# Kernel tuning notes

Hardware: AMD Instinct MI355X
Metric: run time of the kernel (lower is better)

The kernel has to match this reference:

```python
import jax, jax.numpy as jnp
import numpy as np

ALPHA = 0.8
TOPK = 9
LOW_BOUND = 0.0
EPS = 1e-10
IOU_EPS = 1e-6


def pairwise_iou(boxes1, boxes2):
    # boxes1 [N,4], boxes2 [G,4] in x1,y1,x2,y2 -> IoU [N,G] (mmdet BboxOverlaps2D)
    area1 = (boxes1[:, 2] - boxes1[:, 0]) * (boxes1[:, 3] - boxes1[:, 1])  # [N]
    area2 = (boxes2[:, 2] - boxes2[:, 0]) * (boxes2[:, 3] - boxes2[:, 1])  # [G]
    lt = jnp.maximum(boxes1[:, None, :2], boxes2[None, :, :2])  # [N,G,2]
    rb = jnp.minimum(boxes1[:, None, 2:], boxes2[None, :, 2:])  # [N,G,2]
    wh = jnp.clip(rb - lt, 0.0)
    inter = wh[..., 0] * wh[..., 1]  # [N,G]
    union = area1[:, None] + area2[None, :] - inter
    return inter / jnp.maximum(union, IOU_EPS)


def setup_inputs() -> dict:
    key = jax.random.key(0)
    k1, k2, k3, k4, k5, k6, k7 = jax.random.split(key, 7)
    N, G, C = 65536, 256, 80
    IMG = 1024.0
    points = jax.random.uniform(k1, (N, 2), dtype=jnp.float32) * IMG  # (cy, cx)
    p_xy1 = jax.random.uniform(k2, (N, 2), dtype=jnp.float32) * (IMG - 96.0)
    p_wh = jax.random.uniform(k3, (N, 2), dtype=jnp.float32) * 95.0 + 1.0
    bbox_preds = jnp.concatenate([p_xy1, p_xy1 + p_wh], axis=1)  # valid x1y1x2y2
    g_xy1 = jax.random.uniform(k4, (G, 2), dtype=jnp.float32) * (IMG - 256.0)
    g_wh = jax.random.uniform(k5, (G, 2), dtype=jnp.float32) * 255.0 + 1.0
    gt_bboxes = jnp.concatenate([g_xy1, g_xy1 + g_wh], axis=1)
    cls_scores = jax.random.normal(k6, (N, C), dtype=jnp.float32)
    gt_labels = jax.random.randint(k7, (G,), 0, C)
    return {"points": points, "cls_scores": cls_scores, "bbox_preds": bbox_preds,
            "gt_bboxes": gt_bboxes, "gt_labels": gt_labels}


def reference(points, cls_scores, bbox_preds, gt_bboxes, gt_labels):
    num_points = points.shape[0]
    num_gt = gt_bboxes.shape[0]
    overlaps = pairwise_iou(bbox_preds, gt_bboxes)  # [N,G]
    cls_cost = jax.nn.sigmoid(cls_scores[:, gt_labels])  # [N,G]
    overlaps = cls_cost ** (1.0 - ALPHA) * overlaps ** ALPHA
    # top-k points per GT (torch: overlaps.topk(k, dim=0))
    _, topk_idxs = jax.lax.top_k(overlaps.T, TOPK)  # [G,K]
    candidate_idxs = topk_idxs.T  # [K,G]
    cp = jnp.transpose(points[candidate_idxs], (1, 0, 2))  # [G,K,2] (cy,cx)
    # mle_2d_gaussian_2: per-GT MLE Gaussian over candidate points
    miu = cp.mean(axis=1, keepdims=True)  # [G,1,2]
    diff = cp - miu  # [G,K,2]
    sigma = jnp.einsum('gki,gkj->gij', diff, diff) / TOPK  # [G,2,2]
    a, b = sigma[:, 0, 0], sigma[:, 0, 1]
    c, d = sigma[:, 1, 0], sigma[:, 1, 1]
    det = a * d - b * c  # [G]
    inv = jnp.stack([jnp.stack([d, -b], axis=-1),
                     jnp.stack([-c, a], axis=-1)], axis=-2) / (det + EPS)[:, None, None]
    maha = jnp.einsum('gki,gij,gkj->gk', diff, inv, diff)  # [G,K]
    candidate_w = jnp.exp(-0.5 * maha).T  # [K,G]
    # center-inside-gt validity, evaluated only at candidate points
    cy, cx = cp[:, :, 0], cp[:, :, 1]  # [G,K]
    gx1, gy1, gx2, gy2 = (gt_bboxes[:, i][:, None] for i in range(4))  # [G,1]
    valid = ((cx - gx1 > EPS) & (cy - gy1 > EPS) &
             (gx2 - cx > EPS) & (gy2 - cy > EPS)).T  # [K,G]
    wv = candidate_w * valid.astype(candidate_w.dtype)
    # scatter per-GT weights to points, then max over GTs == scatter-max
    w = jnp.zeros((num_points,), dtype=cls_scores.dtype)
    w = w.at[candidate_idxs.reshape(-1)].max(wv.reshape(-1))
    w = jnp.where(w < LOW_BOUND, jnp.zeros_like(w), w)
    return w
```

## Files before the change

kernel.cpp:

```cpp
#include <hip/hip_runtime.h>
#include <hip/hip_bf16.h>
#include <math.h>

#define NPTS   65536
#define NGT    256
#define NCLS   80
#define TOPK   9
#define GSLICE 32
#define NPB    256
#define NXB    (NPTS / NPB)
#define SCAP   64

__device__ inline unsigned long long pack_key(float L, unsigned idx) {
    unsigned u   = __float_as_uint(L);
    unsigned k32 = (u & 0x80000000u) ? ~u : (u | 0x80000000u);
    return ((unsigned long long)k32 << 32) | (unsigned)(~idx);
}

__device__ inline unsigned long long umax64(unsigned long long a,
                                            unsigned long long b) {
    return a > b ? a : b;
}

__device__ inline unsigned long long wave_max64(unsigned long long m) {
#pragma unroll
    for (int off = 1; off < 64; off <<= 1)
        m = umax64(m, (unsigned long long)__shfl_xor(m, off));
    return m;
}

__global__ __launch_bounds__(256) void filter_kernel(
    const float* __restrict__ preds,
    const float* __restrict__ gtb,
    const int*   __restrict__ glab,
    const float* __restrict__ cls,
    unsigned short* __restrict__ counts,
    unsigned long long* __restrict__ bucket,
    float* __restrict__ w)
{
    __shared__ unsigned lcnt[GSLICE];
    __shared__ int      glabs[GSLICE];
    __shared__ unsigned long long stage[GSLICE][SCAP];

    const int t   = threadIdx.x;
    const int xb  = blockIdx.x;
    const int g0  = blockIdx.y * GSLICE;
    const int pt  = xb * NPB + t;
    const int bid = blockIdx.y * NXB + xb;

    if (t < GSLICE) {
        lcnt[t]  = 0u;
        glabs[t] = glab[g0 + t];
    }
    if (t < 32) w[bid * 32 + t] = 0.0f;

    float4 pb = ((const float4*)preds)[pt];
    float parea = (pb.z - pb.x) * (pb.w - pb.y);
    __syncthreads();

    for (int gi = 0; gi < GSLICE; ++gi) {
        const float4 g4 = ((const float4*)gtb)[g0 + gi];
        float ix1 = fmaxf(pb.x, g4.x), iy1 = fmaxf(pb.y, g4.y);
        float ix2 = fminf(pb.z, g4.z), iy2 = fminf(pb.w, g4.w);
        float iw  = fmaxf(ix2 - ix1, 0.0f);
        float ih  = fmaxf(iy2 - iy1, 0.0f);
        float inter = iw * ih;
        if (inter > 0.0f) {
            float garea = (g4.z - g4.x) * (g4.w - g4.y);
            float uni = fmaxf(parea + garea - inter, 1e-6f);
            float iou = inter / uni;
            unsigned long long entry =
                ((unsigned long long)__float_as_uint(iou) << 32) |
                (unsigned)(~(unsigned)pt);
            unsigned slot = atomicAdd(&lcnt[gi], 1u);
            if (slot < SCAP) stage[gi][slot] = entry;
        }
    }
    __syncthreads();

    if (t < GSLICE) {
        unsigned c = lcnt[t];
        if (c > SCAP) c = SCAP;
        lcnt[t] = c;
        counts[(size_t)(g0 + t) * NXB + xb] = (unsigned short)c;
    }
    __syncthreads();

    const float E1 = 1.0f - 0.8f;
#pragma unroll
    for (int k = 0; k < 8; k += 4) {
        unsigned long long e[4];
        bool  vld[4];
        int   gi[4];
        float x[4];
#pragma unroll
        for (int j = 0; j < 4; ++j) {
            int i = (k + j) * 256 + t;
            gi[j] = i >> 6;
            int sl = i & (SCAP - 1);
            e[j]   = stage[gi[j]][sl];
            vld[j] = sl < (int)lcnt[gi[j]];
        }
#pragma unroll
        for (int j = 0; j < 4; ++j) {
            if (vld[j]) {
                unsigned p = ~(unsigned)(e[j] & 0xFFFFFFFFu);
                x[j] = cls[(size_t)p * NCLS + glabs[gi[j]]];
            }
        }
#pragma unroll
        for (int j = 0; j < 4; ++j) {
            if (vld[j]) {
                float iou = __uint_as_float((unsigned)(e[j] >> 32));
                float s   = 1.0f / (1.0f + expf(-x[j]));
                float L   = E1 * log2f(s) + 0.8f * log2f(iou);
                unsigned u   = __float_as_uint(L);
                unsigned k32 = (u & 0x80000000u) ? ~u : (u | 0x80000000u);
                int i = (k + j) * 256 + t;
                bucket[((size_t)(g0 + gi[j]) * NXB + xb) * SCAP + (i & (SCAP - 1))]
                    = ((unsigned long long)k32 << 32) | (e[j] & 0xFFFFFFFFu);
            }
        }
    }
}

__global__ __launch_bounds__(1024) void select_kernel(
    const unsigned short*     __restrict__ counts,
    const unsigned long long* __restrict__ bucket,
    const float* __restrict__ pts,
    const float* __restrict__ gtb,
    float* __restrict__ w)
{
    const int g    = blockIdx.x;
    const int t    = threadIdx.x;
    const int lane = t & 63;
    const int wid  = t >> 6;

    __shared__ unsigned short scnt[NXB];
    __shared__ unsigned long long wl[16 * TOPK];
    __shared__ unsigned tidx[TOPK];
    __shared__ float ppy[TOPK], ppx[TOPK];

    if (t < NXB) scnt[t] = counts[(size_t)g * NXB + t];
    __syncthreads();

    const unsigned long long* src =
        bucket + (size_t)g * (NXB * SCAP) + (size_t)wid * 1024;

    unsigned long long e[16];
#pragma unroll
    for (int k = 0; k < 16; k += 4) {
        unsigned long long v[4];
#pragma unroll
        for (int j = 0; j < 4; ++j) v[j] = src[(k + j) * 64 + lane];
#pragma unroll
        for (int j = 0; j < 4; ++j) {
            int c = (int)scnt[wid * 16 + k + j];
            e[k + j] = (lane < c) ? v[j] : 0ULL;
        }
    }
    unsigned long long mymax = 0ULL;
#pragma unroll
    for (int j = 0; j < 16; ++j) mymax = umax64(mymax, e[j]);

#pragma unroll
    for (int r = 0; r < TOPK; ++r) {
        unsigned long long m = wave_max64(mymax);
        if (lane == 0) wl[wid * TOPK + r] = m;
        if (m != 0ULL && mymax == m) {
#pragma unroll
            for (int j = 0; j < 16; ++j) if (e[j] == m) e[j] = 0ULL;
            mymax = 0ULL;
#pragma unroll
            for (int j = 0; j < 16; ++j) mymax = umax64(mymax, e[j]);
        }
    }
    __syncthreads();

    if (wid == 0) {
        unsigned long long f[4];
        f[0] = wl[lane];
        f[1] = wl[64 + lane];
        f[2] = (lane < 16) ? wl[128 + lane] : 0ULL;
        f[3] = (lane < TOPK) ? pack_key(-INFINITY, (unsigned)lane) : 0ULL;

        unsigned long long mx = 0ULL;
#pragma unroll
        for (int j = 0; j < 4; ++j) mx = umax64(mx, f[j]);

#pragma unroll
        for (int r = 0; r < TOPK; ++r) {
            unsigned long long m = wave_max64(mx);
            if (lane == 0) tidx[r] = ~(unsigned)(m & 0xFFFFFFFFu);
            if (mx == m) {
#pragma unroll
                for (int j = 0; j < 4; ++j) if (f[j] == m) f[j] = 0ULL;
                mx = 0ULL;
#pragma unroll
                for (int j = 0; j < 4; ++j) mx = umax64(mx, f[j]);
            }
        }
    }
    __syncthreads();

    if (t < TOPK) {
        unsigned pi = tidx[t];
        ppy[t] = pts[2 * (size_t)pi];
        ppx[t] = pts[2 * (size_t)pi + 1];
    }
    __syncthreads();

    if (t == 0) {
        float4 g4 = ((const float4*)gtb)[g];
        float m0 = 0.0f, m1 = 0.0f;
#pragma unroll
        for (int k = 0; k < TOPK; ++k) { m0 += ppy[k]; m1 += ppx[k]; }
        m0 /= (float)TOPK; m1 /= (float)TOPK;

        float d0[TOPK], d1[TOPK];
        float a = 0.0f, bb = 0.0f, dd = 0.0f;
#pragma unroll
        for (int k = 0; k < TOPK; ++k) {
            d0[k] = ppy[k] - m0;
            d1[k] = ppx[k] - m1;
            a  += d0[k] * d0[k];
            bb += d0[k] * d1[k];
            dd += d1[k] * d1[k];
        }
        a /= (float)TOPK; bb /= (float)TOPK; dd /= (float)TOPK;
        float det  = a * dd - bb * bb;
        float rinv = 1.0f / (det + 1e-10f);

#pragma unroll
        for (int k = 0; k < TOPK; ++k) {
            float q = d0[k] * (dd * d0[k] - bb * d1[k])
                    + d1[k] * (a  * d1[k] - bb * d0[k]);
            float maha = q * rinv;
            float wt = expf(-0.5f * maha);
            bool valid = (ppx[k] - g4.x > 1e-10f) && (ppy[k] - g4.y > 1e-10f) &&
                         (g4.z - ppx[k] > 1e-10f) && (g4.w - ppy[k] > 1e-10f);
            float wv = valid ? wt : 0.0f;
            atomicMax((int*)&w[tidx[k]], __float_as_int(wv));
        }
    }
}

extern "C" void kernel_launch(void* const* d_in, const int* in_sizes, int n_in,
                              void* d_out, int out_size, void* d_ws, size_t ws_size,
                              hipStream_t stream) {
    const float* points  = (const float*)d_in[0];
    const float* cls     = (const float*)d_in[1];
    const float* preds   = (const float*)d_in[2];
    const float* gtb     = (const float*)d_in[3];
    const int*   glab    = (const int*)d_in[4];
    float* w = (float*)d_out;

    char* ws = (char*)d_ws;
    unsigned long long* bucket = (unsigned long long*)ws;
    size_t off = (size_t)NGT * NXB * SCAP * sizeof(unsigned long long);
    unsigned short* counts = (unsigned short*)(ws + off);

    filter_kernel<<<dim3(NXB, NGT / GSLICE), 256, 0, stream>>>(
        preds, gtb, glab, cls, counts, bucket, w);
    select_kernel<<<NGT, 1024, 0, stream>>>(counts, bucket, points, gtb, w);
}
```

Baseline: 114.6 us.

## Split per-GT top-k selection across four blocks with last-block merge

The select kernel now runs 256-thread blocks, four per ground-truth box, instead of one 1024-thread block per box. Each block picks a local top-9 from a quarter of the buckets and writes it to a workspace buffer. An atomic counter then lets the last-arriving block merge the partial results and compute the Gaussian weights. This raises block count and occupancy for a grid of only 256 blocks, at the cost of extra global traffic, memory fences and an atomic handoff, plus a counter reset done inside the filter kernel.

```diff
diff --git a/kernel.cpp b/kernel.cpp
--- a/kernel.cpp
+++ b/kernel.cpp
@@ -10,6 +10,7 @@
 #define NPB    256
 #define NXB    (NPTS / NPB)
 #define SCAP   64
+#define NSUB   4
 
 __device__ inline unsigned long long pack_key(float L, unsigned idx) {
     unsigned u   = __float_as_uint(L);
@@ -36,6 +37,7 @@
     const float* __restrict__ cls,
     unsigned short* __restrict__ counts,
     unsigned long long* __restrict__ bucket,
+    unsigned* __restrict__ done,
     float* __restrict__ w)
 {
     __shared__ unsigned lcnt[GSLICE];
@@ -51,6 +53,7 @@
     if (t < GSLICE) {
         lcnt[t]  = 0u;
         glabs[t] = glab[g0 + t];
+        if (xb == 0) done[g0 + t] = 0u;
     }
     if (t < 32) w[bid * 32 + t] = 0.0f;
 
@@ -124,38 +127,42 @@
     }
 }
 
-__global__ __launch_bounds__(1024) void select_kernel(
+__global__ __launch_bounds__(256) void select_kernel(
     const unsigned short*     __restrict__ counts,
     const unsigned long long* __restrict__ bucket,
+    unsigned long long*       __restrict__ partial,
+    unsigned*                 __restrict__ done,
     const float* __restrict__ pts,
     const float* __restrict__ gtb,
     float* __restrict__ w)
 {
     const int g    = blockIdx.x;
+    const int sub  = blockIdx.y;
     const int t    = threadIdx.x;
     const int lane = t & 63;
     const int wid  = t >> 6;
 
-    __shared__ unsigned short scnt[NXB];
-    __shared__ unsigned long long wl[16 * TOPK];
+    __shared__ unsigned short scnt[64];
+    __shared__ unsigned long long wl[4 * TOPK];
+    __shared__ int islast_s;
     __shared__ unsigned tidx[TOPK];
     __shared__ float ppy[TOPK], ppx[TOPK];
 
-    if (t < NXB) scnt[t] = counts[(size_t)g * NXB + t];
+    if (t < 64) scnt[t] = counts[(size_t)g * NXB + sub * 64 + t];
     __syncthreads();
 
     const unsigned long long* src =
-        bucket + (size_t)g * (NXB * SCAP) + (size_t)wid * 1024;
+        bucket + (size_t)g * (NXB * SCAP) + (size_t)sub * 4096;
 
     unsigned long long e[16];
 #pragma unroll
     for (int k = 0; k < 16; k += 4) {
         unsigned long long v[4];
 #pragma unroll
-        for (int j = 0; j < 4; ++j) v[j] = src[(k + j) * 64 + lane];
+        for (int j = 0; j < 4; ++j) v[j] = src[(k + j) * 256 + t];
 #pragma unroll
         for (int j = 0; j < 4; ++j) {
-            int c = (int)scnt[wid * 16 + k + j];
+            int c = (int)scnt[(k + j) * 4 + wid];
             e[k + j] = (lane < c) ? v[j] : 0ULL;
         }
     }
@@ -178,26 +185,49 @@
     __syncthreads();
 
     if (wid == 0) {
-        unsigned long long f[4];
-        f[0] = wl[lane];
-        f[1] = wl[64 + lane];
-        f[2] = (lane < 16) ? wl[128 + lane] : 0ULL;
-        f[3] = (lane < TOPK) ? pack_key(-INFINITY, (unsigned)lane) : 0ULL;
-
-        unsigned long long mx = 0ULL;
-#pragma unroll
-        for (int j = 0; j < 4; ++j) mx = umax64(mx, f[j]);
-
+        unsigned long long f0 = (lane < 4 * TOPK) ? wl[lane] : 0ULL;
+        unsigned long long mx = f0;
+        unsigned long long out[TOPK];
+#pragma unroll
+        for (int r = 0; r < TOPK; ++r) {
+            unsigned long long m = wave_max64(mx);
+            out[r] = m;
+            if (m != 0ULL && mx == m) { f0 = 0ULL; mx = 0ULL; }
+            mx = f0;
+        }
+        if (lane == 0) {
+            unsigned long long* dst = partial + ((size_t)g * NSUB + sub) * TOPK;
+#pragma unroll
+            for (int r = 0; r < TOPK; ++r)
+                __hip_atomic_store(&dst[r], out[r], __ATOMIC_RELEASE,
+                                   __HIP_MEMORY_SCOPE_AGENT);
+            __threadfence();
+            unsigned old = atomicAdd(&done[g], 1u);
+            islast_s = (old == NSUB - 1) ? 1 : 0;
+        }
+    }
+    __syncthreads();
+
+    if (!islast_s) return;
+
+    if (wid == 0) {
+        __threadfence();
+        unsigned long long f[2];
+        f[0] = (lane < NSUB * TOPK)
+             ? __hip_atomic_load(&partial[(size_t)g * (NSUB * TOPK) + lane],
+                                 __ATOMIC_ACQUIRE, __HIP_MEMORY_SCOPE_AGENT)
+             : 0ULL;
+        f[1] = (lane < TOPK) ? pack_key(-INFINITY, (unsigned)lane) : 0ULL;
+
+        unsigned long long mx = umax64(f[0], f[1]);
 #pragma unroll
         for (int r = 0; r < TOPK; ++r) {
             unsigned long long m = wave_max64(mx);
             if (lane == 0) tidx[r] = ~(unsigned)(m & 0xFFFFFFFFu);
             if (mx == m) {
 #pragma unroll
-                for (int j = 0; j < 4; ++j) if (f[j] == m) f[j] = 0ULL;
-                mx = 0ULL;
-#pragma unroll
-                for (int j = 0; j < 4; ++j) mx = umax64(mx, f[j]);
+                for (int j = 0; j < 2; ++j) if (f[j] == m) f[j] = 0ULL;
+                mx = umax64(f[0], f[1]);
             }
         }
     }
@@ -259,8 +289,13 @@
     unsigned long long* bucket = (unsigned long long*)ws;
     size_t off = (size_t)NGT * NXB * SCAP * sizeof(unsigned long long);
     unsigned short* counts = (unsigned short*)(ws + off);
+    off += (size_t)NGT * NXB * sizeof(unsigned short);
+    unsigned long long* partial = (unsigned long long*)(ws + off);
+    off += (size_t)NGT * NSUB * TOPK * sizeof(unsigned long long);
+    unsigned* done = (unsigned*)(ws + off);
 
     filter_kernel<<<dim3(NXB, NGT / GSLICE), 256, 0, stream>>>(
-        preds, gtb, glab, cls, counts, bucket, w);
-    select_kernel<<<NGT, 1024, 0, stream>>>(counts, bucket, points, gtb, w);
-}
+        preds, gtb, glab, cls, counts, bucket, done, w);
+    select_kernel<<<dim3(NGT, NSUB), 256, 0, stream>>>(
+        counts, bucket, partial, done, points, gtb, w);
+}
```

Result: slower. 198.1 us (+72.9%).
